# Performance work log

Hardware: AMD Instinct MI355X
Metric: run time of the kernel (lower is better)

Reference implementation:

```python
import jax, jax.numpy as jnp
import numpy as np

S = 7
B = 2
C = 20
STEP = 1.0 / 7
LAMBDA_COORD = 5.0
LAMBDA_NOOBJ = 0.5
EPS = 1e-10


def setup_inputs() -> dict:
    key = jax.random.key(0)
    k1, k2, k3 = jax.random.split(key, 3)
    N = 16384
    pred = jax.random.normal(k1, (N, S, S, 5 * B + C), dtype=jnp.float32)
    target = jax.random.uniform(k2, (N, S, S, 5 * B + C), dtype=jnp.float32)
    # are binary indicators shared across the B target boxes of a cell
    obj = (jax.random.uniform(k3, (N, S, S)) < 0.3).astype(jnp.float32)
    target = target.at[..., 4].set(obj)
    target = target.at[..., 9].set(obj)
    return {"pred": pred, "target": target}


def _convert_boxes(box):
    # box: [N, S, S, B, 4] with (x_off, y_off, w, h); grid col index -> x, row index -> y
    gx = jnp.arange(S, dtype=box.dtype).reshape(1, 1, S, 1)  # dim 2 = x (col)
    gy = jnp.arange(S, dtype=box.dtype).reshape(1, S, 1, 1)  # dim 1 = y (row)
    x0 = (box[..., 0] + gx) * STEP - box[..., 2] / 2
    y0 = (box[..., 1] + gy) * STEP - box[..., 3] / 2
    out = jnp.stack([x0, y0, box[..., 2], box[..., 3]], axis=-1)
    return jnp.clip(out, 0.0)  # torch.clamp(box, 0) clamps all entries


def _pairwise_iou(b1, b2):
    # b1, b2: [N, S, S, B, 4] converted corner-format (x0, y0, w, h); IoU per matched box index
    x1, y1, w1, h1 = b1[..., 0], b1[..., 1], b1[..., 2], b1[..., 3]
    x2, y2, w2, h2 = b2[..., 0], b2[..., 1], b2[..., 2], b2[..., 3]
    inter_w = jnp.clip(w1 + w2 - (jnp.maximum(x1 + w1, x2 + w2) - jnp.minimum(x1, x2)), 0.0)
    inter_h = jnp.clip(h1 + h2 - (jnp.maximum(y1 + h1, y2 + h2) - jnp.minimum(y1, y2)), 0.0)
    inter = inter_w * inter_h
    union = w1 * h1 + w2 * h2 - inter
    return inter / (union + EPS)


def reference(pred, target):
    N = pred.shape[0]
    target_boxes = target[..., : 5 * B].reshape(N, S, S, B, 5)
    pred_boxes = pred[..., : 5 * B].reshape(N, S, S, B, 5)
    target_class = target[..., 5 * B :]
    pred_class = pred[..., 5 * B :]

    # cell has an object if target conf of box index 1 is > 0 (sig_mask in original)
    cell_mask = (target_boxes[..., 1, 4] > 0).astype(pred.dtype)  # [N,S,S]

    ious = _pairwise_iou(
        _convert_boxes(pred_boxes[..., :4]),
        _convert_boxes(target_boxes[..., :4]),
    )  # [N,S,S,B]
    ious = jax.lax.stop_gradient(ious)  # .item() in original detaches the IoU target

    max_i = jnp.argmax(ious, axis=-1)  # responsible box per cell
    resp = jax.nn.one_hot(max_i, B, dtype=pred.dtype)  # [N,S,S,B]

    obj_box = cell_mask[..., None] * resp          # responsible boxes in object cells
    noobj_box = 1.0 - obj_box                      # other box + all boxes in empty cells

    coord_loss = LAMBDA_COORD * jnp.sum(
        obj_box[..., None] * (pred_boxes[..., :4] - target_boxes[..., :4]) ** 2
    )
    conf_loss = jnp.sum(obj_box * (pred_boxes[..., 4] - ious) ** 2)
    noobj_loss = LAMBDA_NOOBJ * jnp.sum(noobj_box * pred_boxes[..., 4] ** 2)
    class_loss = jnp.sum(cell_mask[..., None] * (pred_class - target_class) ** 2)

    return (coord_loss + conf_loss + noobj_loss + class_loss) / N
```

## Files before the change

kernel.cpp:

```cpp
#include <hip/hip_runtime.h>


constexpr int S = 7;
constexpr int FPC = 30;
constexpr int BLK = 256;
constexpr int WAVES = BLK / 64;
constexpr int TILE_F4 = 64 * FPC / 4;
constexpr float STEP = 1.0f / 7.0f;
constexpr float EPS = 1e-10f;

__global__ __launch_bounds__(BLK) void yolo_partial_kernel(
    const float* __restrict__ pred,
    const float* __restrict__ target,
    float* __restrict__ partial) {
  __shared__ float lds[WAVES][64 * FPC];
  __shared__ float wsum[WAVES];

  const int tid = threadIdx.x;
  const int lane = tid & 63;
  const int wid = tid >> 6;
  const int cellw = blockIdx.x * BLK + wid * 64;
  const int cell = cellw + lane;

  float* myld = lds[wid];
  union Buf { float2 v[FPC / 2]; float f[FPC]; };
  Buf P, T;

  {
    const float4* g = (const float4*)(pred + (size_t)cellw * FPC);
    float4* l = (float4*)myld;
    #pragma unroll
    for (int it = 0; it < (TILE_F4 + 63) / 64; ++it) {
      int idx = it * 64 + lane;
      if (idx < TILE_F4) l[idx] = g[idx];
    }
  }
  {
    const float2* l2 = (const float2*)(myld + lane * FPC);
    #pragma unroll
    for (int i = 0; i < FPC / 2; ++i) P.v[i] = l2[i];
  }
  asm volatile("" ::: "memory");
  {
    const float4* g = (const float4*)(target + (size_t)cellw * FPC);
    float4* l = (float4*)myld;
    #pragma unroll
    for (int it = 0; it < (TILE_F4 + 63) / 64; ++it) {
      int idx = it * 64 + lane;
      if (idx < TILE_F4) l[idx] = g[idx];
    }
  }
  {
    const float2* l2 = (const float2*)(myld + lane * FPC);
    #pragma unroll
    for (int i = 0; i < FPC / 2; ++i) T.v[i] = l2[i];
  }

  const float* p = P.f;
  const float* t = T.f;

  const float gx = (float)(cell % S);
  const float gy = (float)((cell / S) % S);
  const float mask = (t[9] > 0.0f) ? 1.0f : 0.0f;

  float iou[2];
  #pragma unroll
  for (int b = 0; b < 2; ++b) {
    const float* pb = p + 5 * b;
    const float* tb = t + 5 * b;
    float px = fmaxf((pb[0] + gx) * STEP - pb[2] * 0.5f, 0.0f);
    float py = fmaxf((pb[1] + gy) * STEP - pb[3] * 0.5f, 0.0f);
    float pw = fmaxf(pb[2], 0.0f);
    float ph = fmaxf(pb[3], 0.0f);
    float tx = fmaxf((tb[0] + gx) * STEP - tb[2] * 0.5f, 0.0f);
    float ty = fmaxf((tb[1] + gy) * STEP - tb[3] * 0.5f, 0.0f);
    float tw = fmaxf(tb[2], 0.0f);
    float th = fmaxf(tb[3], 0.0f);
    float iw = fmaxf(pw + tw - (fmaxf(px + pw, tx + tw) - fminf(px, tx)), 0.0f);
    float ih = fmaxf(ph + th - (fmaxf(py + ph, ty + th) - fminf(py, ty)), 0.0f);
    float inter = iw * ih;
    float uni = pw * ph + tw * th - inter;
    iou[b] = inter / (uni + EPS);
  }
  const int best = (iou[1] > iou[0]) ? 1 : 0;

  float loss = 0.0f;
  #pragma unroll
  for (int b = 0; b < 2; ++b) {
    const float* pb = p + 5 * b;
    const float* tb = t + 5 * b;
    float obj = (b == best) ? mask : 0.0f;
    float d0 = pb[0] - tb[0];
    float d1 = pb[1] - tb[1];
    float d2 = pb[2] - tb[2];
    float d3 = pb[3] - tb[3];
    loss += 5.0f * obj * (d0 * d0 + d1 * d1 + d2 * d2 + d3 * d3);
    float dc = pb[4] - iou[b];
    loss += obj * dc * dc;
    loss += 0.5f * (1.0f - obj) * pb[4] * pb[4];
  }
  float cls = 0.0f;
  #pragma unroll
  for (int k = 10; k < 30; ++k) {
    float d = p[k] - t[k];
    cls += d * d;
  }
  loss += mask * cls;

  #pragma unroll
  for (int off = 32; off > 0; off >>= 1)
    loss += __shfl_down(loss, off, 64);
  if ((tid & 63) == 0) wsum[wid] = loss;
  __syncthreads();
  if (tid == 0) {
    float total = 0.0f;
    #pragma unroll
    for (int w = 0; w < WAVES; ++w) total += wsum[w];
    partial[blockIdx.x] = total;
  }
}

__global__ __launch_bounds__(256) void yolo_reduce_kernel(
    const float* __restrict__ partial, float* __restrict__ out,
    int n, float invN) {
  __shared__ float wsum[4];
  const int tid = threadIdx.x;
  float s = 0.0f;
  for (int i = tid; i < n; i += 256) s += partial[i];
  #pragma unroll
  for (int off = 32; off > 0; off >>= 1)
    s += __shfl_down(s, off, 64);
  if ((tid & 63) == 0) wsum[tid >> 6] = s;
  __syncthreads();
  if (tid == 0)
    out[0] = (wsum[0] + wsum[1] + wsum[2] + wsum[3]) * invN;
}

extern "C" void kernel_launch(void* const* d_in, const int* in_sizes, int n_in,
                              void* d_out, int out_size, void* d_ws, size_t ws_size,
                              hipStream_t stream) {
  const float* pred = (const float*)d_in[0];
  const float* target = (const float*)d_in[1];
  float* out = (float*)d_out;
  float* partial = (float*)d_ws;

  const int ncells = in_sizes[0] / FPC;
  const int nblocks = ncells / BLK;
  const float invN = 1.0f / (float)(ncells / (S * S));

  yolo_partial_kernel<<<nblocks, BLK, 0, stream>>>(pred, target, partial);
  yolo_reduce_kernel<<<1, 256, 0, stream>>>(partial, out, nblocks, invN);
}
```

Before: 206.4 us.

## Use persistent waves with register double-buffered tile prefetch

Replaces the one-block-per-256-cells launch with a fixed grid of 512 persistent blocks whose waves stride over 64-cell tiles. Each wave prefetches the next tile's pred and target into registers while it processes the current tile through LDS, so global loads overlap with compute. Partial sums are now written per wave instead of per block, which drops the block-level barrier. The tile count is hardcoded to the test cell count, and holding four 8-entry float4 buffers raises register pressure and can lower occupancy.

```diff
diff --git a/kernel.cpp b/kernel.cpp
--- a/kernel.cpp
+++ b/kernel.cpp
@@ -4,61 +4,56 @@
 constexpr int S = 7;
 constexpr int FPC = 30;
 constexpr int BLK = 256;
-constexpr int WAVES = BLK / 64;
+constexpr int NBLOCKS = 512;
+constexpr int NWAVES = NBLOCKS * (BLK / 64);
 constexpr int TILE_F4 = 64 * FPC / 4;
+constexpr int NTILES = 802816 / 64;
 constexpr float STEP = 1.0f / 7.0f;
 constexpr float EPS = 1e-10f;
 
-__global__ __launch_bounds__(BLK) void yolo_partial_kernel(
-    const float* __restrict__ pred,
-    const float* __restrict__ target,
-    float* __restrict__ partial) {
-  __shared__ float lds[WAVES][64 * FPC];
-  __shared__ float wsum[WAVES];
+__device__ __forceinline__ void issue_tile(const float* __restrict__ pred,
+                                           const float* __restrict__ target,
+                                           int tile, int lane,
+                                           float4* rp, float4* rt) {
+  const float4* gp = (const float4*)(pred + (size_t)tile * 64 * FPC);
+  const float4* gt = (const float4*)(target + (size_t)tile * 64 * FPC);
+  #pragma unroll
+  for (int i = 0; i < 8; ++i) {
+    int idx = i * 64 + lane;
+    if (idx < TILE_F4) {
+      rp[i] = gp[idx];
+      rt[i] = gt[idx];
+    }
+  }
+}
 
-  const int tid = threadIdx.x;
-  const int lane = tid & 63;
-  const int wid = tid >> 6;
-  const int cellw = blockIdx.x * BLK + wid * 64;
-  const int cell = cellw + lane;
-
-  float* myld = lds[wid];
+__device__ __forceinline__ float process_tile(float* myld, int tile, int lane,
+                                              const float4* rp, const float4* rt) {
+  float4* l4 = (float4*)myld;
   union Buf { float2 v[FPC / 2]; float f[FPC]; };
   Buf P, T;
+  const float2* l2 = (const float2*)(myld + lane * FPC);
 
-  {
-    const float4* g = (const float4*)(pred + (size_t)cellw * FPC);
-    float4* l = (float4*)myld;
-    #pragma unroll
-    for (int it = 0; it < (TILE_F4 + 63) / 64; ++it) {
-      int idx = it * 64 + lane;
-      if (idx < TILE_F4) l[idx] = g[idx];
-    }
+  #pragma unroll
+  for (int i = 0; i < 8; ++i) {
+    int idx = i * 64 + lane;
+    if (idx < TILE_F4) l4[idx] = rp[i];
   }
-  {
-    const float2* l2 = (const float2*)(myld + lane * FPC);
-    #pragma unroll
-    for (int i = 0; i < FPC / 2; ++i) P.v[i] = l2[i];
+  #pragma unroll
+  for (int i = 0; i < FPC / 2; ++i) P.v[i] = l2[i];
+  asm volatile("" ::: "memory");
+  #pragma unroll
+  for (int i = 0; i < 8; ++i) {
+    int idx = i * 64 + lane;
+    if (idx < TILE_F4) l4[idx] = rt[i];
   }
+  #pragma unroll
+  for (int i = 0; i < FPC / 2; ++i) T.v[i] = l2[i];
   asm volatile("" ::: "memory");
-  {
-    const float4* g = (const float4*)(target + (size_t)cellw * FPC);
-    float4* l = (float4*)myld;
-    #pragma unroll
-    for (int it = 0; it < (TILE_F4 + 63) / 64; ++it) {
-      int idx = it * 64 + lane;
-      if (idx < TILE_F4) l[idx] = g[idx];
-    }
-  }
-  {
-    const float2* l2 = (const float2*)(myld + lane * FPC);
-    #pragma unroll
-    for (int i = 0; i < FPC / 2; ++i) T.v[i] = l2[i];
-  }
 
   const float* p = P.f;
   const float* t = T.f;
-
+  const int cell = tile * 64 + lane;
   const float gx = (float)(cell % S);
   const float gy = (float)((cell / S) % S);
   const float mask = (t[9] > 0.0f) ? 1.0f : 0.0f;
@@ -106,18 +101,45 @@
     cls += d * d;
   }
   loss += mask * cls;
+  return loss;
+}
+
+__global__ __launch_bounds__(BLK) void yolo_partial_kernel(
+    const float* __restrict__ pred,
+    const float* __restrict__ target,
+    float* __restrict__ partial) {
+  __shared__ float lds[BLK / 64][64 * FPC];
+
+  const int tid = threadIdx.x;
+  const int lane = tid & 63;
+  const int wid = tid >> 6;
+  const int gw = blockIdx.x * (BLK / 64) + wid;
+  float* myld = lds[wid];
+
+  float4 Ap[8], At[8], Bp[8], Bt[8];
+  float acc = 0.0f;
+
+  int tile = gw;
+  bool more = (tile < NTILES);
+  if (more) issue_tile(pred, target, tile, lane, Ap, At);
+  while (more) {
+    int nxt = tile + NWAVES;
+    bool moreB = (nxt < NTILES);
+    if (moreB) issue_tile(pred, target, nxt, lane, Bp, Bt);
+    acc += process_tile(myld, tile, lane, Ap, At);
+    if (!moreB) break;
+    int nxt2 = nxt + NWAVES;
+    bool moreA = (nxt2 < NTILES);
+    if (moreA) issue_tile(pred, target, nxt2, lane, Ap, At);
+    acc += process_tile(myld, nxt, lane, Bp, Bt);
+    tile = nxt2;
+    more = moreA;
+  }
 
   #pragma unroll
   for (int off = 32; off > 0; off >>= 1)
-    loss += __shfl_down(loss, off, 64);
-  if ((tid & 63) == 0) wsum[wid] = loss;
-  __syncthreads();
-  if (tid == 0) {
-    float total = 0.0f;
-    #pragma unroll
-    for (int w = 0; w < WAVES; ++w) total += wsum[w];
-    partial[blockIdx.x] = total;
-  }
+    acc += __shfl_down(acc, off, 64);
+  if (lane == 0) partial[gw] = acc;
 }
 
 __global__ __launch_bounds__(256) void yolo_reduce_kernel(
@@ -145,9 +167,8 @@
   float* partial = (float*)d_ws;
 
   const int ncells = in_sizes[0] / FPC;
-  const int nblocks = ncells / BLK;
   const float invN = 1.0f / (float)(ncells / (S * S));
 
-  yolo_partial_kernel<<<nblocks, BLK, 0, stream>>>(pred, target, partial);
-  yolo_reduce_kernel<<<1, 256, 0, stream>>>(partial, out, nblocks, invN);
+  yolo_partial_kernel<<<NBLOCKS, BLK, 0, stream>>>(pred, target, partial);
+  yolo_reduce_kernel<<<1, 256, 0, stream>>>(partial, out, NWAVES, invN);
 }
```

After: 254.3 us. +23.2%, slower.
